# Optimization experiments

Hardware: AMD Instinct MI355X
Metric: run time of the kernel (lower is better)

## Reference

```python
import jax, jax.numpy as jnp
from jax import lax
import numpy as np

D = 1024   # d_model
N = 64     # d_state
P = 64     # headdim
H = 16     # nheads = d_inner // headdim (d_inner = d_model)
E = 8      # n_experts
R = 8      # LoRA rank
OM = 32    # omega_dim
MEMD = 384 # memory vector dim
KC = 4     # d_conv
Bz, Lz = 2, 1024


def setup_inputs() -> dict:
    key = jax.random.key(0)
    it = iter(jax.random.split(key, 48))
    def nrm(shape, s=0.02):
        return jax.random.normal(next(it), shape, jnp.float32) * s
    return dict(
        x=jax.random.normal(next(it), (Bz, Lz, D), jnp.float32),
        wkv_state=nrm((Bz, N, N), 0.1),
        x_prev=jax.random.normal(next(it), (Bz, 1, D), jnp.float32),
        memory_vec=jax.random.normal(next(it), (Bz, MEMD), jnp.float32),
        rag_state=nrm((Bz, N, N), 0.1),
        ssd_state=nrm((Bz, H, P, N), 0.1),
        conv_state=nrm((Bz, D, KC), 0.1),
        norm_scale=jnp.ones((D,), jnp.float32), norm_bias=jnp.zeros((D,), jnp.float32),
        W_in=nrm((2 * D, D)), conv_w=nrm((D, KC), 0.1), conv_b=jnp.zeros((D,), jnp.float32),
        W_dt=nrm((H, D)), dt_bias=jnp.full((H,), -2.0, jnp.float32),
        A_log=jnp.log(jnp.linspace(0.5, 8.0, H)).astype(jnp.float32),
        W_B=nrm((N, D)), W_C=nrm((N, D)), W_ssd_out=nrm((D, D)),
        W_r=nrm((N, D)), W_k=nrm((N, D)), W_v=nrm((N, D)), W_w=nrm((N, D)),
        W_rwkv_out=nrm((D, N)),
        W_skew=nrm((OM, OM), 0.1), W_om_in=nrm((OM, D)), W_om_out=nrm((D, OM)),
        W_router=nrm((E, D)), lora_A=nrm((E, D, R)), lora_B=nrm((E, R, D)),
        W_nov=nrm((1, 2 * D)), b_nov=jnp.zeros((1,), jnp.float32),
        W_ragq=nrm((N, D)), W_rago=nrm((D, N)),
        W_mq=nrm((MEMD, D)), W_mp=nrm((D, MEMD)),
        W_mg=nrm((1, D + MEMD)), b_mg=jnp.zeros((1,), jnp.float32),
    )


def _layernorm(x, s, b):
    m = x.mean(-1, keepdims=True)
    v = ((x - m) ** 2).mean(-1, keepdims=True)
    return (x - m) * lax.rsqrt(v + 1e-5) * s + b


def _forward(x, wkv_state, x_prev, memory_vec, rag_state, ssd_state, conv_state,
             norm_scale, norm_bias, W_in, conv_w, conv_b, W_dt, dt_bias, A_log,
             W_B, W_C, W_ssd_out, W_r, W_k, W_v, W_w, W_rwkv_out,
             W_skew, W_om_in, W_om_out, W_router, lora_A, lora_B, W_nov, b_nov,
             W_ragq, W_rago, W_mq, W_mp, W_mg, b_mg):
    Bb, Ll, _ = x.shape
    residual = x
    xn = _layernorm(x, norm_scale, norm_bias)
    # ---- TarsCoreBlock: Mamba-2 SSD scan + RWKV-7 wkv scan + gated fusion ----
    zu = xn @ W_in.T
    z, u = zu[..., :D], zu[..., D:]
    # depthwise causal conv1d with rolling conv_state [B, D, KC]
    u_cat = jnp.concatenate([conv_state.transpose(0, 2, 1), u], axis=1)  # [B, KC+L, D]
    acc = conv_b
    for k in range(KC):
        acc = acc + u_cat[:, k:k + Ll, :] * conv_w[:, k]
    uc = jax.nn.silu(acc)
    conv_new = u_cat[:, Ll:, :].transpose(0, 2, 1)
    dt = jax.nn.softplus(xn @ W_dt.T + dt_bias)   # [B,L,H]
    A = -jnp.exp(A_log)                            # [H], negative decay rates
    Bm = xn @ W_B.T                                # [B,L,N]
    Cm = xn @ W_C.T                                # [B,L,N]
    uh = uc.reshape(Bb, Ll, H, P)
    def ssd_step(h, inp):
        dt_t, u_t, b_t, c_t = inp                  # [B,H],[B,H,P],[B,N],[B,N]
        h = h * jnp.exp(dt_t * A)[..., None, None] + (dt_t[..., None, None] * u_t[..., None]) * b_t[:, None, None, :]
        return h, jnp.einsum('bhpn,bn->bhp', h, c_t)
    ssd_new, ys = lax.scan(ssd_step, ssd_state,
                           (dt.transpose(1, 0, 2), uh.transpose(1, 0, 2, 3),
                            Bm.transpose(1, 0, 2), Cm.transpose(1, 0, 2)))
    y_ssd = ys.transpose(1, 0, 2, 3).reshape(Bb, Ll, D) @ W_ssd_out.T
    # RWKV-7 style wkv recurrence with time-shift mixing
    x_shift = jnp.concatenate([x_prev, xn[:, :-1]], axis=1)
    mix = 0.5 * (xn + x_shift)
    r, kk, v = mix @ W_r.T, mix @ W_k.T, mix @ W_v.T
    w = jnp.exp(-jnp.exp(mix @ W_w.T))             # per-channel decay in (0,1)
    def rwkv_step(S, inp):
        r_t, k_t, v_t, w_t = inp
        S = S * w_t[:, :, None] + v_t[:, :, None] * k_t[:, None, :]
        return S, jnp.einsum('bij,bj->bi', S, r_t)
    wkv_new, yr = lax.scan(rwkv_step, wkv_state,
                           (r.transpose(1, 0, 2), kk.transpose(1, 0, 2),
                            v.transpose(1, 0, 2), w.transpose(1, 0, 2)))
    y_rwkv = yr.transpose(1, 0, 2) @ W_rwkv_out.T
    core_out = jax.nn.silu(z) * y_ssd + y_rwkv     # WuNeng fusion
    x1 = residual + core_out
    x_prev_new = xn[:, -1:, :]
    # ---- RAG injection from compressed rag_state ----
    q = x1.mean(1) @ W_ragq.T                      # [B,N]
    info = jnp.einsum('bij,bj->bi', rag_state, q)
    x1 = x1 + 0.1 * (info @ W_rago.T)[:, None, :]
    # ---- Omega-SSM: Cayley SO(n) rotation in omega subspace ----
    Ask = 0.5 * (W_skew - W_skew.T)
    I = jnp.eye(OM, dtype=x.dtype)
    Qc = jnp.linalg.solve(I - Ask, I + Ask)        # orthogonal via Cayley map
    x1 = x1 + ((x1 @ W_om_in.T) @ Qc.T) @ W_om_out.T
    # ---- MoLE: sparse top-2 low-rank (LoRA) experts ----
    probs = jax.nn.softmax(x1 @ W_router.T, axis=-1)  # [B,L,E]
    _, topi = lax.top_k(probs, 2)
    mask = jax.nn.one_hot(topi, E, dtype=x.dtype).sum(-2)
    gate = probs * mask
    gate = gate / (gate.sum(-1, keepdims=True) + 1e-9)
    down = jnp.einsum('bld,edr->bler', x1, lora_A)    # [B,L,E,R]
    x2 = x1 + jnp.einsum('bler,erd->bld', down * gate[..., None], lora_B)
    aux = E * jnp.sum(probs.mean((0, 1)) * mask.mean((0, 1)))
    # ---- NoveltyGate blended residual ----
    h_old, h_new = residual.mean(1), x2.mean(1)
    novelty = jax.nn.sigmoid(jnp.concatenate([h_old, h_new], -1) @ W_nov.T + b_nov)[:, 0]
    n = novelty[:, None, None]
    x3 = n * x2 + (1.0 - n) * residual
    # ---- Cosine-gated memory fusion ----
    h_post = x3.mean(1)
    hq = h_post @ W_mq.T
    sim = (hq * memory_vec).sum(-1) / (jnp.linalg.norm(hq, axis=-1) * jnp.linalg.norm(memory_vec, axis=-1) + 1e-8)
    gm = jax.nn.sigmoid(jnp.concatenate([h_post, memory_vec], -1) @ W_mg.T + b_mg)[:, 0]
    x4 = x3 + (sim * gm)[:, None, None] * (memory_vec @ W_mp.T)[:, None, :]
    return x4, wkv_new, x_prev_new, ssd_new, conv_new, aux


def reference(x, wkv_state, x_prev, memory_vec, rag_state, ssd_state, conv_state,
              norm_scale, norm_bias, W_in, conv_w, conv_b, W_dt, dt_bias, A_log,
              W_B, W_C, W_ssd_out, W_r, W_k, W_v, W_w, W_rwkv_out,
              W_skew, W_om_in, W_om_out, W_router, lora_A, lora_B, W_nov, b_nov,
              W_ragq, W_rago, W_mq, W_mp, W_mg, b_mg):
    return _forward(x, wkv_state, x_prev, memory_vec, rag_state, ssd_state, conv_state,
                    norm_scale, norm_bias, W_in, conv_w, conv_b, W_dt, dt_bias, A_log,
                    W_B, W_C, W_ssd_out, W_r, W_k, W_v, W_w, W_rwkv_out,
                    W_skew, W_om_in, W_om_out, W_router, lora_A, lora_B, W_nov, b_nov,
                    W_ragq, W_rago, W_mq, W_mp, W_mg, b_mg)
```

## Files before the change

kernel.cpp:

```cpp
#include <hip/hip_runtime.h>
#include <hip/hip_bf16.h>

#define DD    1024
#define NN    64
#define HH    16
#define EE    8
#define OMM   32
#define MEMDD 384
#define BB    2
#define LL    1024
#define TT    2048

#define OFF_X4    0
#define OFF_WKV   2097152
#define OFF_XPREV 2105344
#define OFF_SSD   2107392
#define OFF_CONV  2238464
#define OFF_AUX   2246656

typedef unsigned short u16;
typedef __attribute__((ext_vector_type(8))) short short8;
typedef __attribute__((ext_vector_type(4))) float f32x4;

__device__ __forceinline__ float us2f(u16 u){ return __uint_as_float(((unsigned)u)<<16); }
__device__ __forceinline__ u16 f2us(float f){
    unsigned u = __float_as_uint(f);
    unsigned r = 0x7FFFu + ((u>>16)&1u);
    return (u16)((u + r) >> 16);
}
__device__ __forceinline__ float LD(const void* p, size_t i, int m){
    return m ? ((const float*)p)[i] : us2f(((const u16*)p)[i]);
}
__device__ __forceinline__ void ST(void* p, size_t i, float v, int m){
    if (m) ((float*)p)[i] = v; else ((u16*)p)[i] = f2us(v);
}
__device__ __forceinline__ float sigf(float x){ return 1.f/(1.f+expf(-x)); }

__device__ __forceinline__ void gl_lds16(const u16* g, u16* l){
    __builtin_amdgcn_global_load_lds((const __attribute__((address_space(1))) void*)g,
                                     (__attribute__((address_space(3))) void*)l,
                                     16, 0, 0);
}

__device__ __forceinline__ float wave_sum64(float v){
    #pragma unroll
    for (int off=32; off>0; off>>=1) v += __shfl_xor(v, off);
    return v;
}
__device__ __forceinline__ float block_sum256(float v, float* red){
    int tid = threadIdx.x;
    red[tid] = v; __syncthreads();
    #pragma unroll
    for (int st=128; st>0; st>>=1){ if (tid<st) red[tid]+=red[tid+st]; __syncthreads(); }
    float r = red[0]; __syncthreads();
    return r;
}
__device__ __forceinline__ int detect_mode(const void* nscale){
    return (((const unsigned*)nscale)[0] == 0x3F800000u) ? 1 : 0;
}
__device__ __forceinline__ void cvt8(const void* src, size_t i, u16* dst, int md){
    if (md){
        float4 a = *(const float4*)((const float*)src + i);
        float4 b = *(const float4*)((const float*)src + i + 4);
        dst[0]=f2us(a.x); dst[1]=f2us(a.y); dst[2]=f2us(a.z); dst[3]=f2us(a.w);
        dst[4]=f2us(b.x); dst[5]=f2us(b.y); dst[6]=f2us(b.z); dst[7]=f2us(b.w);
    } else {
        *(short8*)dst = *(const short8*)((const u16*)src + i);
    }
}

__global__ __launch_bounds__(256)
void prep_k(const void* nscale, int* flag, float* mean1, float* hold, float* hnew,
            const void* W_in, u16* wbfin,
            const void* W_ssd_out, u16* wbfss,
            const void* W_rwkv_out, u16* wbfrw,
            const void* WB, const void* WC, const void* Wdt, u16* wcatxn,
            const void* Wr, const void* Wk, const void* Wv, const void* Ww, u16* wcatmix,
            const void* memv, const void* W_mp, float* mdel){
    __shared__ float mv[MEMDD];
    const int md = detect_mode(nscale);
    int bx = blockIdx.x, tid = threadIdx.x;
    switch (blockIdx.y){
    case 0: {
        size_t i = (size_t)bx*2048 + tid*8;
        cvt8(W_in, i, wbfin + i, md);
    } break;
    case 1: {
        if (bx >= 512) return;
        size_t i = (size_t)bx*2048 + tid*8;
        cvt8(W_ssd_out, i, wbfss + i, md);
    } break;
    case 2: {
        if (bx >= 32) return;
        size_t i = (size_t)bx*2048 + tid*8;
        cvt8(W_rwkv_out, i, wbfrw + i, md);
    } break;
    case 3: {
        if (bx >= 72) return;
        const void* src; size_t off;
        if (bx < 32){ src = WB; off = (size_t)bx*2048; }
        else if (bx < 64){ src = WC; off = (size_t)(bx-32)*2048; }
        else { src = Wdt; off = (size_t)(bx-64)*2048; }
        size_t dsto = (bx < 32) ? off : (bx < 64 ? 65536 + off : 131072 + off);
        cvt8(src, off + tid*8, wcatxn + dsto + tid*8, md);
    } break;
    case 4: {
        if (bx >= 128) return;
        int sel = bx >> 5;
        const void* src = (sel==0)?Wr:(sel==1)?Wk:(sel==2)?Wv:Ww;
        size_t off = (size_t)(bx & 31)*2048 + tid*8;
        cvt8(src, off, wcatmix + (size_t)sel*65536 + off, md);
    } break;
    case 5: {
        if (bx >= 64) return;
        int b = bx & 1, r0 = (bx >> 1)*32;
        int wid = tid >> 6, lane = tid & 63;
        for (int i=tid; i<MEMDD; i+=256) mv[i] = LD(memv, b*MEMDD + i, md);
        __syncthreads();
        #pragma unroll
        for (int rr=0; rr<8; ++rr){
            int row = r0 + wid*8 + rr;
            float s = 0.f;
            size_t wo = (size_t)row*MEMDD;
            #pragma unroll
            for (int it=0; it<6; ++it) s += LD(W_mp, wo + it*64 + lane, md) * mv[it*64 + lane];
            s = wave_sum64(s);
            if (lane == 0) mdel[b*DD + row] = s;
        }
    } break;
    default: {
        if (bx >= 8) return;
        int t = bx*256 + tid;
        if (t == 0) flag[0] = md;
        if (t < BB*DD){ mean1[t]=0.f; hold[t]=0.f; hnew[t]=0.f; }
    } break;
    }
}

__global__ __launch_bounds__(256)
void ln_k(const void* __restrict__ x, const void* __restrict__ scale, const void* __restrict__ bias,
          float* __restrict__ xn, u16* __restrict__ xnbf, void* __restrict__ out, const int* modep){
    __shared__ float red[256];
    const int m = *modep;
    int t = blockIdx.x, tid = threadIdx.x;
    int b = t >> 10, l = t & 1023;
    float v[4]; float s=0.f;
    #pragma unroll
    for (int i=0;i<4;i++){ v[i] = LD(x, (size_t)t*DD + i*256 + tid, m); s += v[i]; }
    float mean = block_sum256(s, red) * (1.f/DD);
    float s2=0.f;
    #pragma unroll
    for (int i=0;i<4;i++){ float d=v[i]-mean; s2 += d*d; }
    float var = block_sum256(s2, red) * (1.f/DD);
    float rstd = rsqrtf(var + 1e-5f);
    #pragma unroll
    for (int i=0;i<4;i++){
        int d = i*256+tid;
        float o = (v[i]-mean)*rstd*LD(scale,d,m) + LD(bias,d,m);
        xn[(size_t)t*DD + d] = o;
        xnbf[(size_t)t*DD + d] = f2us(o);
        if (l == LL-1) ST(out, OFF_XPREV + b*DD + d, o, m);
    }
}

__device__ __forceinline__ void gemm_body(u16* Asm, u16* Bsm,
                const u16* __restrict__ A, const u16* __restrict__ W,
                float* __restrict__ C0, float* __restrict__ C1,
                int N, int K, int Nsplit, int addto, int c0bf, int bx, int by){
    int tid = threadIdx.x;
    int wid = tid >> 6, lane = tid & 63;
    int l15 = lane & 15, quad = lane >> 4;
    int wr = wid >> 1, wc = wid & 1;
    int bm = bx*64, bn = by*128;
    int lr = lane >> 3;
    int lc8 = (lane & 7)*8;
    const u16* Ag = A + (size_t)bm*K;
    const u16* Wg = W + (size_t)bn*K;
    f32x4 acc[2][4];
    #pragma unroll
    for (int m=0;m<2;++m)
        #pragma unroll
        for (int n=0;n<4;++n) acc[m][n] = (f32x4){0.f,0.f,0.f,0.f};
    for (int k0=0; k0<K; k0+=64){
        #pragma unroll
        for (int i=0;i<2;++i){
            int row = wid*16 + i*8 + lr;
            gl_lds16(Ag + (size_t)row*K + k0 + lc8, &Asm[(wid*16 + i*8)*64]);
        }
        #pragma unroll
        for (int i=0;i<4;++i){
            int row = wid*32 + i*8 + lr;
            gl_lds16(Wg + (size_t)row*K + k0 + lc8, &Bsm[(wid*32 + i*8)*64]);
        }
        __syncthreads();
        #pragma unroll
        for (int ks=0; ks<2; ++ks){
            short8 af[2], bf[4];
            #pragma unroll
            for (int m=0;m<2;++m)
                af[m] = *(const short8*)&Asm[(wr*32 + m*16 + l15)*64 + ks*32 + quad*8];
            #pragma unroll
            for (int n=0;n<4;++n)
                bf[n] = *(const short8*)&Bsm[(wc*64 + n*16 + l15)*64 + ks*32 + quad*8];
            #pragma unroll
            for (int m=0;m<2;++m)
                #pragma unroll
                for (int n=0;n<4;++n)
                    acc[m][n] = __builtin_amdgcn_mfma_f32_16x16x32_bf16(af[m], bf[n], acc[m][n], 0,0,0);
        }
        __syncthreads();
    }
    int ns1 = N - Nsplit;
    #pragma unroll
    for (int m=0;m<2;++m){
        #pragma unroll
        for (int n=0;n<4;++n){
            int col = bn + wc*64 + n*16 + l15;
            #pragma unroll
            for (int i=0;i<4;++i){
                int row = bm + wr*32 + m*16 + quad*4 + i;
                float v = acc[m][n][i];
                if (col < Nsplit){
                    size_t id = (size_t)row*Nsplit + col;
                    if (c0bf) ((u16*)C0)[id] = f2us(v);
                    else C0[id] = (addto ? C0[id] : 0.f) + v;
                } else {
                    size_t id = (size_t)row*ns1 + (col - Nsplit);
                    C1[id] = v;
                }
            }
        }
    }
}

__global__ __launch_bounds__(256)
void gemm_big_k(const u16* __restrict__ A, const u16* __restrict__ W,
                float* __restrict__ C0, float* __restrict__ C1,
                int N, int K, int Nsplit, int addto){
    __shared__ u16 Asm[64*64];
    __shared__ u16 Bsm[128*64];
    gemm_body(Asm, Bsm, A, W, C0, C1, N, K, Nsplit, addto, 0, blockIdx.x, blockIdx.y);
}

__global__ __launch_bounds__(256)
void proj_dual_k(const u16* __restrict__ xnbf, const u16* __restrict__ wcatxn,
                 float* __restrict__ pcat2_as_f, float* __restrict__ dtraw,
                 const u16* __restrict__ mixbf, const u16* __restrict__ wcatmix,
                 float* __restrict__ rkvw){
    __shared__ u16 Asm[64*64];
    __shared__ u16 Bsm[128*64];
    if (blockIdx.y < 2)
        gemm_body(Asm, Bsm, xnbf, wcatxn, pcat2_as_f, dtraw, 256, 1024, 128, 0, 1, blockIdx.x, blockIdx.y);
    else
        gemm_body(Asm, Bsm, mixbf, wcatmix, rkvw, dtraw, 256, 1024, 256, 0, 0, blockIdx.x, blockIdx.y-2);
}

__global__ __launch_bounds__(256)
void out_dual_k(const u16* __restrict__ ysbf, const u16* __restrict__ wbfss, float* __restrict__ s1,
                const u16* __restrict__ ybf, const u16* __restrict__ wbfrw, float* __restrict__ s2){
    __shared__ u16 Asm[64*64];
    __shared__ u16 Bsm[128*64];
    if (blockIdx.y < 8)
        gemm_body(Asm, Bsm, ysbf, wbfss, s1, (float*)nullptr, 1024, 1024, 1024, 0, 0, blockIdx.x, blockIdx.y);
    else
        gemm_body(Asm, Bsm, ybf, wbfrw, s2, (float*)nullptr, 1024, 64, 1024, 0, 0, blockIdx.x, blockIdx.y-8);
}

__global__ __launch_bounds__(256)
void cmx_k(const float* __restrict__ u, const float* __restrict__ xn,
           const void* __restrict__ cs, const void* __restrict__ cw, const void* __restrict__ cb,
           const void* __restrict__ xprev,
           float* __restrict__ uc, u16* __restrict__ mixbf, void* __restrict__ out,
           const int* modep){
    const int m = *modep;
    int idx = blockIdx.x*256 + threadIdx.x;
    int t = idx >> 10, d = idx & 1023;
    int b = t >> 10, l = t & 1023;
    float acc = LD(cb, d, m);
    #pragma unroll
    for (int k=0;k<4;++k){
        int i = l + k;
        float xv = (i < 4) ? LD(cs, ((size_t)(b*DD + d))*4 + i, m)
                           : u[(size_t)(t + k - 4)*DD + d];
        acc += xv * LD(cw, d*4 + k, m);
    }
    uc[idx] = acc * sigf(acc);
    float xc = xn[idx];
    float xp = (l == 0) ? LD(xprev, (size_t)b*DD + d, m) : xn[idx - DD];
    mixbf[idx] = f2us(0.5f*(xc + xp));
    if (l >= LL-4)
        ST(out, OFF_CONV + (size_t)b*DD*4 + d*4 + (l - (LL-4)), u[idx], m);
}

#define LDSS 72
__global__ __launch_bounds__(256)
void ssdA_k(const u16* __restrict__ pcat2, const float* __restrict__ dtraw,
            const float* __restrict__ uc,
            const void* __restrict__ A_log, const void* __restrict__ dt_bias,
            float* __restrict__ ys, float* __restrict__ Scb, float* __restrict__ cumsb,
            const int* modep){
    __shared__ u16 Bs[64*LDSS];
    __shared__ u16 Cs[64*LDSS];
    __shared__ u16 BTw[64*LDSS];
    __shared__ u16 XTs[64*LDSS];
    __shared__ float cums[64];
    __shared__ float dts_raw[64];
    const int m = *modep;
    int tid = threadIdx.x;
    int wid = tid >> 6, lane = tid & 63;
    int blk = blockIdx.x;
    int b = blk >> 8, h = (blk >> 4) & 15, c = blk & 15;
    int l16 = lane & 15, quad = lane >> 4;
    int r = tid >> 2;
    int cb4 = (tid & 3) * 16;
    float Ah = -expf(LD(A_log, h, m));
    int t0 = c*64;
    const u16* Pg = pcat2 + (size_t)(b*LL + t0)*128;
    #pragma unroll
    for (int i=0;i<4;++i){
        int cc = cb4 + i*4;
        ushort4 f = *(const ushort4*)(Pg + (size_t)r*128 + cc);
        u16* d1 = &Bs[r*LDSS + cc];
        d1[0]=f.x; d1[1]=f.y; d1[2]=f.z; d1[3]=f.w;
        ushort4 g = *(const ushort4*)(Pg + (size_t)r*128 + 64 + cc);
        u16* d2 = &Cs[r*LDSS + cc];
        d2[0]=g.x; d2[1]=g.y; d2[2]=g.z; d2[3]=g.w;
    }
// ... 52 lines not shown
        for (int i=0;i<4;++i){
            int t_loc = wid*16 + quad*4 + i;
            float gv = (s_loc <= t_loc) ? gacc[nt][i]*expf(cums[t_loc]-cums[s_loc]) : 0.f;
            Bs[t_loc*LDSS + s_loc] = f2us(gv);
        }
    }
    __syncthreads();
    f32x4 acc2[4], acc4[4];
    #pragma unroll
    for (int nt=0;nt<4;++nt){ acc2[nt]=(f32x4){0.f,0.f,0.f,0.f}; acc4[nt]=(f32x4){0.f,0.f,0.f,0.f}; }
    #pragma unroll
    for (int ks=0; ks<64; ks+=32){
        short8 sf = *(const short8*)&Bs[(wid*16 + l16)*LDSS + ks + quad*8];
        short8 xf = *(const short8*)&XTs[(wid*16 + l16)*LDSS + ks + quad*8];
        #pragma unroll
        for (int nt=0;nt<4;++nt){
            short8 xo = *(const short8*)&XTs[(nt*16 + l16)*LDSS + ks + quad*8];
            acc2[nt] = __builtin_amdgcn_mfma_f32_16x16x32_bf16(sf, xo, acc2[nt], 0,0,0);
            short8 bo = *(const short8*)&BTw[(nt*16 + l16)*LDSS + ks + quad*8];
            acc4[nt] = __builtin_amdgcn_mfma_f32_16x16x32_bf16(xf, bo, acc4[nt], 0,0,0);
        }
    }
    #pragma unroll
    for (int nt=0;nt<4;++nt){
        int col = nt*16 + l16;
        #pragma unroll
        for (int i=0;i<4;++i){
            int row = wid*16 + quad*4 + i;
            ys[(size_t)(b*LL + t0 + row)*DD + h*64 + col] = acc2[nt][i];
            Scb[(size_t)blk*4096 + row*64 + col] = acc4[nt][i];
        }
    }
}

#define FS 68
__global__ __launch_bounds__(256)
void rwkvA_k(const float* __restrict__ rkvw,
             float* __restrict__ yr, float* __restrict__ Slb, float* __restrict__ Wcumb){
    __shared__ float wch[64*FS], vch[64*FS], kch[64*FS], rch[64*FS];
    __shared__ float Wc[64*FS];
    __shared__ float part[4*8*64];
    int tid = threadIdx.x;
    int wid = tid >> 6, lane = tid & 63;
    int blk = blockIdx.x;
    int b = blk >> 4, c = blk & 15;
    int t0 = c*64;
    int r = tid >> 2, c4 = (tid & 3)*16;
    const float* base = rkvw + (size_t)(b*LL + t0)*256;
    #pragma unroll
    for (int i=0;i<4;++i){
        int cc = c4 + i*4;
        *(float4*)&rch[r*FS+cc] = *(const float4*)(base + (size_t)r*256 + cc);
        *(float4*)&kch[r*FS+cc] = *(const float4*)(base + (size_t)r*256 + 64 + cc);
        *(float4*)&vch[r*FS+cc] = *(const float4*)(base + (size_t)r*256 + 128 + cc);
        float4 wv = *(const float4*)(base + (size_t)r*256 + 192 + cc);
        wch[r*FS+cc+0] = expf(-expf(wv.x));
        wch[r*FS+cc+1] = expf(-expf(wv.y));
        wch[r*FS+cc+2] = expf(-expf(wv.z));
        wch[r*FS+cc+3] = expf(-expf(wv.w));
    }
    __syncthreads();
    if (wid == 0){
        float cum = 1.f;
        for (int t=0;t<64;++t){ cum *= wch[t*FS+lane]; Wc[t*FS+lane] = cum; }
    }
    __syncthreads();
    #pragma unroll
    for (int q=0;q<16;++q){
        int idx = q*256 + tid;
        int t = idx >> 6, i = idx & 63;
        Wcumb[(size_t)blk*4096 + idx] = Wc[t*FS + i];
    }
    float S[16];
    #pragma unroll
    for (int jj=0;jj<16;++jj) S[jj]=0.f;
    int jb = wid*16;
    for (int t8=0; t8<8; ++t8){
        float ya[8];
        #pragma unroll
        for (int u=0;u<8;++u){
            int t = t8*8+u;
            float wv = wch[t*FS+lane];
            float vv = vch[t*FS+lane];
            float y = 0.f;
            #pragma unroll
            for (int jj=0;jj<16;++jj){
                float kk = kch[t*FS + jb + jj];
                float rr = rch[t*FS + jb + jj];
                S[jj] = S[jj]*wv + vv*kk;
                y += S[jj]*rr;
            }
            ya[u] = y;
        }
        #pragma unroll
        for (int u=0;u<8;++u) part[wid*512 + u*64 + lane] = ya[u];
        __syncthreads();
        #pragma unroll
        for (int it=0; it<2; ++it){
            int e = it*256 + tid;
            int u = e >> 6, i = e & 63;
            float y = part[0*512 + u*64 + i] + part[1*512 + u*64 + i]
                    + part[2*512 + u*64 + i] + part[3*512 + u*64 + i];
            yr[(size_t)(b*LL + t0 + t8*8 + u)*NN + i] = y;
        }
        __syncthreads();
    }
    #pragma unroll
    for (int jj=0;jj<16;++jj)
        Slb[(size_t)blk*4096 + (size_t)lane*64 + jb + jj] = S[jj];
}

__global__ __launch_bounds__(256)
void sb_k(const void* __restrict__ ssd_state, const float* __restrict__ Scb,
          const float* __restrict__ cumsb, u16* __restrict__ hinb,
          const void* __restrict__ wkv_state, const float* __restrict__ Slb,
          const float* __restrict__ Wcumb, u16* __restrict__ hinr,
          void* __restrict__ out, const int* modep){
    const int m = *modep;
    int tid = threadIdx.x;
    if (blockIdx.x < 32){
        int bh = blockIdx.x;
        float h[16];
        #pragma unroll
        for (int i=0;i<16;++i)
            h[i] = LD(ssd_state, (size_t)bh*4096 + i*256 + tid, m);
        for (int c=0; c<16; ++c){
            int blk = bh*16 + c;
            float efull = expf(cumsb[(size_t)blk*64 + 63]);
            #pragma unroll
            for (int i=0;i<16;++i){
                hinb[(size_t)blk*4096 + i*256 + tid] = f2us(h[i]);
                h[i] = efull*h[i] + Scb[(size_t)blk*4096 + i*256 + tid];
            }
        }
        #pragma unroll
        for (int i=0;i<16;++i)
            ST(out, OFF_SSD + (size_t)bh*4096 + i*256 + tid, h[i], m);
    } else {
        int b = blockIdx.x - 32;
        float S[16];
        #pragma unroll
        for (int q=0;q<16;++q)
            S[q] = LD(wkv_state, (size_t)b*4096 + q*256 + tid, m);
        for (int c=0;c<16;++c){
            int blk = b*16+c;
            #pragma unroll
            for (int q=0;q<16;++q){
                int idx = q*256+tid;
                int i = idx >> 6;
                hinr[(size_t)blk*4096 + idx] = f2us(S[q]);
                float P = Wcumb[(size_t)blk*4096 + 63*64 + i];
                S[q] = S[q]*P + Slb[(size_t)blk*4096 + idx];
            }
        }
        #pragma unroll
        for (int q=0;q<16;++q)
            ST(out, OFF_WKV + (size_t)b*4096 + q*256 + tid, S[q], m);
    }
}

__global__ __launch_bounds__(256)
void sc_k(const u16* __restrict__ pcat2, const u16* __restrict__ hinb,
          const float* __restrict__ cumsb, const float* __restrict__ ys, u16* __restrict__ ysbf,
          const float* __restrict__ rkvw, const u16* __restrict__ hinr,
          const float* __restrict__ Wcumb, const float* __restrict__ yr, u16* __restrict__ ybf){
    __shared__ u16 T0[64*LDSS];
    __shared__ u16 T1[64*LDSS];
    int tid = threadIdx.x;
    int wid = tid >> 6, lane = tid & 63;
    int l16 = lane & 15, quad = lane >> 4;
    int r = tid >> 2;
    int cb4 = (tid & 3)*16;
    if (blockIdx.x < 512){
        int blk = blockIdx.x;
        int b = blk >> 8, h = (blk >> 4) & 15, c = blk & 15;
// ... 76 lines not shown
}

__global__ __launch_bounds__(256)
void fuse_mean_k(const float* __restrict__ z, const float* __restrict__ s1,
                 const float* __restrict__ s2, const void* __restrict__ xin,
                 float* __restrict__ x1, float* __restrict__ mean1, const int* modep){
    const int m = *modep;
    int bid = blockIdx.x;
    int lc = bid & 15, dc = (bid >> 4) & 3, b = bid >> 6;
    int d = dc*256 + threadIdx.x;
    float sum = 0.f;
    int l0 = lc*64;
    for (int l=l0; l<l0+64; ++l){
        size_t idx = (size_t)(b*LL + l)*DD + d;
        float zl = z[idx];
        float v = LD(xin, idx, m) + zl*sigf(zl)*s1[idx] + s2[idx];
        x1[idx] = v;
        sum += v;
    }
    atomicAdd(&mean1[b*DD + d], sum*(1.f/LL));
}

__global__ __launch_bounds__(256)
void ragA_k(const float* __restrict__ mean1, const void* __restrict__ W_ragq,
            float* __restrict__ qb, const int* modep){
    const int m = *modep;
    int bx = blockIdx.x;
    int b = bx >> 4;
    int tid = threadIdx.x, wid = tid >> 6, lane = tid & 63;
    int row = (bx & 15)*4 + wid;
    float s = 0.f;
    size_t wo = (size_t)row*DD;
    #pragma unroll
    for (int it=0; it<16; ++it)
        s += LD(W_ragq, wo + it*64 + lane, m) * mean1[(b<<10) + it*64 + lane];
    s = wave_sum64(s);
    if (lane == 0) qb[b*64 + row] = s;
}

__global__ __launch_bounds__(256)
void ragB_k(const float* __restrict__ qb, const void* __restrict__ rag_state,
            float* __restrict__ infob, const int* modep){
    const int m = *modep;
    int bx = blockIdx.x;
    int b = bx >> 4;
    int tid = threadIdx.x, wid = tid >> 6, lane = tid & 63;
    int row = (bx & 15)*4 + wid;
    float s = LD(rag_state, (size_t)(b*64+row)*64 + lane, m) * qb[b*64 + lane];
    s = wave_sum64(s);
    if (lane == 0) infob[b*64 + row] = s;
}

__global__ __launch_bounds__(256)
void ragC_k(const float* __restrict__ infob, const void* __restrict__ W_rago,
            float* __restrict__ ragd, const int* modep){
    const int m = *modep;
    int bx = blockIdx.x;
    int b = bx >> 6;
    int tid = threadIdx.x, wid = tid >> 6, lane = tid & 63;
    int r0 = (bx & 63)*16 + wid*4;
    float iv = infob[b*64 + lane];
    #pragma unroll
    for (int rr=0; rr<4; ++rr){
        int d = r0 + rr;
        float s = iv * LD(W_rago, (size_t)d*64 + lane, m);
        s = wave_sum64(s);
        if (lane == 0) ragd[(b<<10) + d] = 0.1f*s;
    }
}

__global__ __launch_bounds__(256)
void addrag_k(float* __restrict__ x1, const float* __restrict__ ragd, u16* __restrict__ xbf){
    int i4 = (blockIdx.x*256 + threadIdx.x)*4;
    int b = i4 >> 20, d = i4 & 1023;
    #pragma unroll
    for (int j=0;j<4;++j){
        float v = x1[i4+j] + ragd[(b<<10) + d + j];
        x1[i4+j] = v;
        xbf[i4+j] = f2us(v);
    }
}

__global__ __launch_bounds__(256)
void cayley_k(const void* __restrict__ W_skew, float* __restrict__ Qc, const int* modep){
    __shared__ float Aug[32][65];
    __shared__ float fac[32];
    const int m = *modep;
    int tid = threadIdx.x;
    for (int idx = tid; idx < 1024; idx += 256){
        int r = idx >> 5, c = idx & 31;
        float a = 0.5f*(LD(W_skew, r*32+c, m) - LD(W_skew, c*32+r, m));
        float eye = (r==c) ? 1.f : 0.f;
        Aug[r][c] = eye - a;
        Aug[r][32+c] = eye + a;
    }
    __syncthreads();
    for (int p=0; p<32; ++p){
        float inv = 1.f / Aug[p][p];
        __syncthreads();
        if (tid < 64) Aug[p][tid] *= inv;
        if (tid < 32 && tid != p) fac[tid] = Aug[tid][p];
        __syncthreads();
        for (int idx = tid; idx < 2048; idx += 256){
            int r = idx >> 6, c = idx & 63;
            if (r != p) Aug[r][c] -= fac[r]*Aug[p][c];
        }
        __syncthreads();
    }
    for (int idx = tid; idx < 1024; idx += 256){
        int r = idx >> 5, c = idx & 31;
        Qc[idx] = Aug[r][32+c];
    }
}

__global__ __launch_bounds__(256)
void wcomb2_k(const void* __restrict__ W_om_out, const float* __restrict__ Qc,
              const void* __restrict__ W_om_in, u16* __restrict__ wcomb, const int* modep){
    const int md = *modep;
    int d = blockIdx.x;
    int tid = threadIdx.x;
    __shared__ float qc[1024];
    __shared__ float wrow[32];
    __shared__ float trow[32];
    #pragma unroll
    for (int i=0;i<4;i++) qc[i*256+tid] = Qc[i*256+tid];
    if (tid < 32) wrow[tid] = LD(W_om_out, (size_t)d*OMM + tid, md);
    __syncthreads();
    if (tid < 32){
        float s = 0.f;
        #pragma unroll
        for (int j=0;j<32;++j) s += wrow[j]*qc[j*32 + tid];
        trow[tid] = s;
    }
    __syncthreads();
    #pragma unroll
    for (int p=0; p<4; ++p){
        int e = p*256 + tid;
        float s = 0.f;
        #pragma unroll
        for (int k=0; k<32; ++k) s += trow[k] * LD(W_om_in, (size_t)k*DD + e, md);
        wcomb[(size_t)d*DD + e] = f2us(s);
    }
}

__global__ __launch_bounds__(256)
void moe_k(const float* __restrict__ x1, const void* __restrict__ W_router,
           const void* __restrict__ lora_A, const void* __restrict__ lora_B,
           float* __restrict__ x2, float* __restrict__ probs8, int* __restrict__ eidx,
           const int* modep){
    const int m = *modep;
    int t = blockIdx.x, tid = threadIdx.x;
    int wid = tid >> 6, lane = tid & 63;
    __shared__ float xs[1024];
    __shared__ float red[32];
    __shared__ float logits[8];
    __shared__ float downs[16];
    __shared__ float gsh[2];
    __shared__ int esh[2];
    #pragma unroll
    for (int i=0;i<4;i++) xs[i*256+tid] = x1[(size_t)t*DD + i*256+tid];
    __syncthreads();
    {
        float p0=0.f, p1=0.f;
        size_t w0o = (size_t)(2*wid)*DD, w1o = (size_t)(2*wid+1)*DD;
        #pragma unroll
        for (int it=0; it<16; ++it){
            float xv = xs[it*64 + lane];
            p0 += xv * LD(W_router, w0o + it*64 + lane, m);
            p1 += xv * LD(W_router, w1o + it*64 + lane, m);
        }
        p0 = wave_sum64(p0); p1 = wave_sum64(p1);
        if (lane == 0){ logits[2*wid] = p0; logits[2*wid+1] = p1; }
    }
    __syncthreads();
    if (tid == 0){
        float mx = logits[0];
        for (int e2=1;e2<8;++e2) mx = fmaxf(mx, logits[e2]);
        float pe[8]; float sum=0.f;
        for (int e2=0;e2<8;++e2){ pe[e2]=expf(logits[e2]-mx); sum+=pe[e2]; }
        for (int e2=0;e2<8;++e2) pe[e2] /= sum;
        int e0=0; for (int e2=1;e2<8;++e2) if (pe[e2]>pe[e0]) e0=e2;
        int e1=(e0==0)?1:0; for (int e2=0;e2<8;++e2) if (e2!=e0 && pe[e2]>pe[e1]) e1=e2;
        float gs = pe[e0]+pe[e1]+1e-9f;
        gsh[0]=pe[e0]/gs; gsh[1]=pe[e1]/gs; esh[0]=e0; esh[1]=e1;
        #pragma unroll
        for (int e2=0;e2<8;++e2) probs8[(size_t)t*8 + e2] = pe[e2];
        eidx[t*2+0]=e0; eidx[t*2+1]=e1;
    }
    __syncthreads();
    {
        int ei = wid & 1, half = wid >> 1;
        int e2 = esh[ei];
        int dsub = lane >> 3;
        size_t ao = (size_t)e2*8192 + (size_t)half*4096;
        float acc = 0.f;
        #pragma unroll
        for (int c=0; c<64; ++c){
            float xv = xs[half*512 + c*8 + dsub];
            acc += xv * LD(lora_A, ao + c*64 + lane, m);
        }
        acc += __shfl_xor(acc, 8);
        acc += __shfl_xor(acc, 16);
        acc += __shfl_xor(acc, 32);
        if (lane < 8) red[wid*8 + lane] = acc;
    }
    __syncthreads();
    if (tid < 16){
        int ei = tid >> 3, r = tid & 7;
        downs[ei*8 + r] = red[ei*8 + r] + red[(ei+2)*8 + r];
    }
    __syncthreads();
    {
        int e0=esh[0], e1=esh[1]; float g0=gsh[0], g1=gsh[1];
        #pragma unroll
        for (int i=0;i<4;i++){
            int d = i*256+tid;
            float acc=0.f;
            size_t b0 = (size_t)e0*8192 + d;
            size_t b1 = (size_t)e1*8192 + d;
            #pragma unroll
            for (int r=0;r<8;++r) acc += g0*downs[r]*LD(lora_B, b0 + (size_t)r*1024, m)
                                       + g1*downs[8+r]*LD(lora_B, b1 + (size_t)r*1024, m);
            x2[(size_t)t*DD + d] = xs[d] + acc;
        }
    }
}

__global__ __launch_bounds__(256)
void colmean2_k(const float* __restrict__ x2, const void* __restrict__ xin,
                float* __restrict__ hnew, float* __restrict__ hold, const int* modep){
    const int m = *modep;
    int bid = blockIdx.x;
    int lc = bid & 15, dc = (bid >> 4) & 3, b = bid >> 6;
    int d = dc*256 + threadIdx.x;
    float s = 0.f;
    int l0 = lc*64;
    if (blockIdx.y == 0){
        for (int l=l0; l<l0+64; ++l) s += x2[(size_t)(b*LL + l)*DD + d];
        atomicAdd(&hnew[b*DD + d], s*(1.f/LL));
    } else {
        for (int l=l0; l<l0+64; ++l) s += LD(xin, (size_t)(b*LL + l)*DD + d, m);
        atomicAdd(&hold[b*DD + d], s*(1.f/LL));
    }
}

__global__ __launch_bounds__(256)
void hq2_k(const float* __restrict__ hold, const float* __restrict__ hnew,
           const void* __restrict__ W_nov, const void* __restrict__ b_nov,
           const void* __restrict__ W_mq, float* __restrict__ hqb, const int* modep){
    const int m = *modep;
    int b = blockIdx.x, tid = threadIdx.x;
    int wid = tid >> 6, lane = tid & 63;
    int r0 = blockIdx.y*16;
    __shared__ float hs[1024];
    __shared__ float red[256];
    float p=0.f;
    #pragma unroll
    for (int i=0;i<4;i++){ int d=i*256+tid;
        p += hold[b*DD+d]*LD(W_nov,d,m) + hnew[b*DD+d]*LD(W_nov,DD+d,m); }
    float n = sigf(block_sum256(p, red) + LD(b_nov,0,m));
    #pragma unroll
    for (int i=0;i<4;i++){ int d=i*256+tid;
        hs[d] = n*hnew[b*DD+d] + (1.f-n)*hold[b*DD+d]; }
    __syncthreads();
    #pragma unroll
    for (int rr=0; rr<4; ++rr){
        int row = r0 + wid*4 + rr;
        float s = 0.f;
        size_t wo = (size_t)row*DD;
        #pragma unroll
        for (int it=0; it<16; ++it) s += LD(W_mq, wo + it*64 + lane, m) * hs[it*64 + lane];
        s = wave_sum64(s);
        if (lane == 0) hqb[b*MEMDD + row] = s;
    }
}

__global__ __launch_bounds__(256)
void gate2_k(const float* __restrict__ hold, const float* __restrict__ hnew,
             const void* __restrict__ W_nov, const void* __restrict__ b_nov,
             const float* __restrict__ hqb, const void* __restrict__ memv,
             const void* __restrict__ W_mg, const void* __restrict__ b_mg,
             const float* __restrict__ probs8, const int* __restrict__ eidx,
             float* __restrict__ scal, void* __restrict__ out, const int* modep){
    const int m = *modep;
    int b = blockIdx.x, tid = threadIdx.x;
    __shared__ float red[256];
    float p=0.f;
    #pragma unroll
    for (int i=0;i<4;i++){ int d=i*256+tid;
        p += hold[b*DD+d]*LD(W_nov,d,m) + hnew[b*DD+d]*LD(W_nov,DD+d,m); }
    float n = sigf(block_sum256(p, red) + LD(b_nov,0,m));
    float pn=0.f, ph=0.f, pm=0.f;
    for (int mm=tid; mm<MEMDD; mm+=256){
        float mv = LD(memv, b*MEMDD+mm, m);
        float h = hqb[b*MEMDD+mm];
        pn += h*mv; ph += h*h; pm += mv*mv;
    }
    float num = block_sum256(pn, red);
    float nh  = block_sum256(ph, red);
    float nm  = block_sum256(pm, red);
    float sim = num / (sqrtf(nh)*sqrtf(nm) + 1e-8f);
    float pg=0.f;
    #pragma unroll
    for (int i=0;i<4;i++){ int d=i*256+tid;
        float hp = n*hnew[b*DD+d] + (1.f-n)*hold[b*DD+d];
        pg += hp*LD(W_mg,d,m); }
    for (int mm=tid; mm<MEMDD; mm+=256) pg += LD(memv,b*MEMDD+mm,m)*LD(W_mg,DD+mm,m);
    float gdot = block_sum256(pg, red) + LD(b_mg,0,m);
    float gm = sigf(gdot);
    if (tid==0){ scal[b] = n; scal[2+b] = sim*gm; }
    if (b == 0){
        float ps[8] = {0.f,0.f,0.f,0.f,0.f,0.f,0.f,0.f};
        float cs[8] = {0.f,0.f,0.f,0.f,0.f,0.f,0.f,0.f};
        for (int t=tid; t<TT; t+=256){
            #pragma unroll
            for (int e=0;e<8;++e) ps[e] += probs8[(size_t)t*8 + e];
            int e0 = eidx[t*2], e1 = eidx[t*2+1];
            #pragma unroll
            for (int e=0;e<8;++e) cs[e] += (e0==e ? 1.f : 0.f) + (e1==e ? 1.f : 0.f);
        }
        float aux = 0.f;
        #pragma unroll
        for (int e=0;e<8;++e){
            float sp = block_sum256(ps[e], red);
            float sc = block_sum256(cs[e], red);
            aux += (sp*(1.f/TT))*(sc*(1.f/TT));
        }
        if (tid==0) ST(out, OFF_AUX, 8.f*aux, m);
    }
}

__global__ __launch_bounds__(256)
void final_k(const float* __restrict__ x2, const void* __restrict__ xin,
             const float* __restrict__ scal, const float* __restrict__ mdelta,
             void* __restrict__ out, const int* modep){
    const int m = *modep;
    int i4 = (blockIdx.x*256 + threadIdx.x)*4;
    int b = i4 >> 20, d = i4 & 1023;
    float n = scal[b], coef = scal[2+b];
    #pragma unroll
    for (int j=0;j<4;++j){
        float v = n*x2[i4+j] + (1.f-n)*LD(xin,i4+j,m) + coef*mdelta[(b<<10)+d+j];
        ST(out, OFF_X4 + i4 + j, v, m);
    }
}

extern "C" void kernel_launch(void* const* d_in, const int* in_sizes, int n_in,
                              void* d_out, int out_size, void* d_ws, size_t ws_size,
                              hipStream_t stream){
    typedef const void* cb;
    cb x         = d_in[0];
    cb wkv_state = d_in[1];
    cb x_prev    = d_in[2];
    cb memv      = d_in[3];
    cb rag_state = d_in[4];
    cb ssd_state = d_in[5];
    cb conv_state= d_in[6];
    cb nscale    = d_in[7];
    cb nbias     = d_in[8];
    cb W_in      = d_in[9];
    cb conv_w    = d_in[10];
    cb conv_b    = d_in[11];
    cb W_dt      = d_in[12];
    cb dt_bias   = d_in[13];
    cb A_log     = d_in[14];
    cb W_B       = d_in[15];
    cb W_C       = d_in[16];
    cb W_ssd_out = d_in[17];
    cb W_r       = d_in[18];
    cb W_k       = d_in[19];
    cb W_v       = d_in[20];
    cb W_w       = d_in[21];
    cb W_rwkv_out= d_in[22];
    cb W_skew    = d_in[23];
    cb W_om_in   = d_in[24];
    cb W_om_out  = d_in[25];
    cb W_router  = d_in[26];
    cb lora_A    = d_in[27];
    cb lora_B    = d_in[28];
    cb W_nov     = d_in[29];
    cb b_nov     = d_in[30];
    cb W_ragq    = d_in[31];
    cb W_rago    = d_in[32];
    cb W_mq      = d_in[33];
    cb W_mp      = d_in[34];
    cb W_mg      = d_in[35];
    cb b_mg      = d_in[36];

    float* ws = (float*)d_ws;
    size_t o = 0;
    float* xn_x1   = ws + o; o += (size_t)TT*DD;
    float* z_x2    = ws + o; o += (size_t)TT*DD;
    float* u_ys    = ws + o; o += (size_t)TT*DD;
    float* ucb     = ws + o; o += (size_t)TT*DD;
    float* s2b     = ws + o; o += (size_t)TT*DD;
    float* dtraw   = ws + o; o += (size_t)TT*128;
    float* rkvw    = ws + o; o += (size_t)TT*256;
    float* yrb     = ws + o; o += (size_t)TT*NN;
    float* Qcb     = ws + o; o += 1024;
    float* Scb     = ws + o; o += (size_t)512*4096;
    float* cumsb   = ws + o; o += (size_t)512*64;
    float* Wcumb   = ws + o; o += (size_t)32*4096;
    float* Slb     = ws + o; o += (size_t)32*4096;
    u16*   hinb    = (u16*)(ws + o); o += (size_t)512*4096/2;
    u16*   hinr    = (u16*)(ws + o); o += (size_t)32*4096/2;
    float* mean1   = ws + o; o += BB*DD;
    float* ragd    = ws + o; o += BB*DD;
    float* qb      = ws + o; o += BB*NN;
    float* infob   = ws + o; o += BB*NN;
    float* holdb   = ws + o; o += BB*DD;
    float* hnewb   = ws + o; o += BB*DD;
    float* scal    = ws + o; o += 16;
    float* mdel    = ws + o; o += BB*DD;
    float* hqb     = ws + o; o += BB*MEMDD;
    float* probs8  = ws + o; o += (size_t)TT*8;
    int*   eidx    = (int*)(ws + o); o += (size_t)TT*2;
    int*   flag    = (int*)(ws + o); o += 16;
    u16*   xnbf    = (u16*)(ws + o); o += (size_t)TT*DD/2;
    u16*   mixbf   = (u16*)(ws + o); o += (size_t)TT*DD/2;
    u16*   x1bf    = (u16*)(ws + o); o += (size_t)TT*DD/2;
    u16*   ysbf    = (u16*)(ws + o); o += (size_t)TT*DD/2;
    u16*   ybf     = (u16*)(ws + o); o += (size_t)TT*NN/2;
    u16*   pcat2   = (u16*)(ws + o); o += (size_t)TT*128/2;
    u16*   wbfin   = (u16*)(ws + o); o += (size_t)2*DD*DD/2;
    u16*   wbfss   = (u16*)(ws + o); o += (size_t)DD*DD/2;
    u16*   wbfrw   = (u16*)(ws + o); o += (size_t)DD*NN/2;
    u16*   wcatxn  = (u16*)(ws + o); o += (size_t)256*DD/2;
    u16*   wcatmix = (u16*)(ws + o); o += (size_t)256*DD/2;
    u16*   wcombbf = (u16*)(ws + o); o += (size_t)DD*DD/2;

    dim3 blk(256);

    hipLaunchKernelGGL(prep_k, dim3(1024,7), blk, 0, stream,
                       nscale, flag, mean1, holdb, hnewb,
                       W_in, wbfin, W_ssd_out, wbfss, W_rwkv_out, wbfrw,
                       W_B, W_C, W_dt, wcatxn, W_r, W_k, W_v, W_w, wcatmix,
                       memv, W_mp, mdel);
    hipLaunchKernelGGL(cayley_k, dim3(1), blk, 0, stream, W_skew, Qcb, flag);
    hipLaunchKernelGGL(wcomb2_k, dim3(1024), blk, 0, stream, W_om_out, Qcb, W_om_in, wcombbf, flag);
    hipLaunchKernelGGL(ln_k, dim3(TT), blk, 0, stream, x, nscale, nbias, xn_x1, xnbf, d_out, flag);
    hipLaunchKernelGGL(gemm_big_k, dim3(TT/64, 16), blk, 0, stream, xnbf, wbfin,
                       z_x2, u_ys, 2*DD, DD, DD, 0);
    hipLaunchKernelGGL(cmx_k, dim3(TT*DD/256), blk, 0, stream, u_ys, xn_x1,
                       conv_state, conv_w, conv_b, x_prev, ucb, mixbf, d_out, flag);
    hipLaunchKernelGGL(proj_dual_k, dim3(TT/64, 4), blk, 0, stream,
                       xnbf, wcatxn, (float*)pcat2, dtraw, mixbf, wcatmix, rkvw);
    hipLaunchKernelGGL(ssdA_k, dim3(512), blk, 0, stream, pcat2, dtraw, ucb, A_log, dt_bias,
                       u_ys , Scb, cumsb, flag);
    hipLaunchKernelGGL(rwkvA_k, dim3(32), blk, 0, stream, rkvw, yrb, Slb, Wcumb);
    hipLaunchKernelGGL(sb_k, dim3(34), blk, 0, stream, ssd_state, Scb, cumsb, hinb,
                       wkv_state, Slb, Wcumb, hinr, d_out, flag);
    hipLaunchKernelGGL(sc_k, dim3(544), blk, 0, stream, pcat2, hinb, cumsb, u_ys, ysbf,
                       rkvw, hinr, Wcumb, yrb, ybf);
    hipLaunchKernelGGL(out_dual_k, dim3(TT/64, 16), blk, 0, stream,
                       ysbf, wbfss, ucb , ybf, wbfrw, s2b);
    hipLaunchKernelGGL(fuse_mean_k, dim3(128), blk, 0, stream, z_x2, ucb, s2b, x,
                       xn_x1 , mean1, flag);
    hipLaunchKernelGGL(ragA_k, dim3(32), blk, 0, stream, mean1, W_ragq, qb, flag);
    hipLaunchKernelGGL(ragB_k, dim3(32), blk, 0, stream, qb, rag_state, infob, flag);
    hipLaunchKernelGGL(ragC_k, dim3(128), blk, 0, stream, infob, W_rago, ragd, flag);
    hipLaunchKernelGGL(addrag_k, dim3(TT*DD/1024), blk, 0, stream, xn_x1, ragd, x1bf);
    hipLaunchKernelGGL(gemm_big_k, dim3(TT/64, 8), blk, 0, stream, x1bf, wcombbf,
                       xn_x1, (float*)nullptr, DD, DD, DD, 1);
    hipLaunchKernelGGL(moe_k, dim3(TT), blk, 0, stream, xn_x1, W_router, lora_A, lora_B, z_x2,
                       probs8, eidx, flag);
    hipLaunchKernelGGL(colmean2_k, dim3(128,2), blk, 0, stream, z_x2, x, hnewb, holdb, flag);
    hipLaunchKernelGGL(hq2_k, dim3(BB,24), blk, 0, stream, holdb, hnewb, W_nov, b_nov,
                       W_mq, hqb, flag);
    hipLaunchKernelGGL(gate2_k, dim3(BB), blk, 0, stream, holdb, hnewb, W_nov, b_nov,
                       hqb, memv, W_mg, b_mg, probs8, eidx, scal, d_out, flag);
    hipLaunchKernelGGL(final_k, dim3(TT*DD/1024), blk, 0, stream, z_x2, x, scal, mdel, d_out, flag);
}
```

Measured before the change: 474.9 us.

## Fold Cayley and wcomb into prep/LN kernels, add 128x128 input GEMM

The single-block Cayley inverse moves into prep_k as an extra grid row, and the wcomb computation is appended to ln_k as extra blocks, which removes two kernel launches. The input projection switches to a new 128x128-tile MFMA GEMM that gets more reuse per loaded tile. The RWKV inner loop is split into four independent accumulators to shorten the dependency chain, and the aux-loss reduction uses wave reductions in place of sixteen block reductions. Putting the serial Cayley solve inside prep_k may lengthen that kernel's tail, and the larger GEMM tiles launch fewer blocks.

After: 461.5 us. 1.03x faster.

```diff
diff --git a/kernel.cpp b/kernel.cpp
--- a/kernel.cpp
+++ b/kernel.cpp
@@ -76,8 +76,11 @@
             const void* W_rwkv_out, u16* wbfrw,
             const void* WB, const void* WC, const void* Wdt, u16* wcatxn,
             const void* Wr, const void* Wk, const void* Wv, const void* Ww, u16* wcatmix,
-            const void* memv, const void* W_mp, float* mdel){
+            const void* memv, const void* W_mp, float* mdel,
+            const void* W_skew, float* Qc){
     __shared__ float mv[MEMDD];
+    __shared__ float Aug[32][65];
+    __shared__ float fac[32];
     const int md = detect_mode(nscale);
     int bx = blockIdx.x, tid = threadIdx.x;
     switch (blockIdx.y){
@@ -128,6 +131,33 @@
             if (lane == 0) mdel[b*DD + row] = s;
         }
     } break;
+    case 6: {
+        if (bx >= 1) return;
+        for (int idx = tid; idx < 1024; idx += 256){
+            int r = idx >> 5, c = idx & 31;
+            float a = 0.5f*(LD(W_skew, r*32+c, md) - LD(W_skew, c*32+r, md));
+            float eye = (r==c) ? 1.f : 0.f;
+            Aug[r][c] = eye - a;
+            Aug[r][32+c] = eye + a;
+        }
+        __syncthreads();
+        for (int p=0; p<32; ++p){
+            float inv = 1.f / Aug[p][p];
+            __syncthreads();
+            if (tid < 64) Aug[p][tid] *= inv;
+            if (tid < 32 && tid != p) fac[tid] = Aug[tid][p];
+            __syncthreads();
+            for (int idx = tid; idx < 2048; idx += 256){
+                int r = idx >> 6, c = idx & 63;
+                if (r != p) Aug[r][c] -= fac[r]*Aug[p][c];
+            }
+            __syncthreads();
+        }
+        for (int idx = tid; idx < 1024; idx += 256){
+            int r = idx >> 5, c = idx & 31;
+            Qc[idx] = Aug[r][32+c];
+        }
+    } break;
     default: {
         if (bx >= 8) return;
         int t = bx*256 + tid;
@@ -139,10 +169,40 @@
 
 __global__ __launch_bounds__(256)
 void ln_k(const void* __restrict__ x, const void* __restrict__ scale, const void* __restrict__ bias,
-          float* __restrict__ xn, u16* __restrict__ xnbf, void* __restrict__ out, const int* modep){
+          float* __restrict__ xn, u16* __restrict__ xnbf, void* __restrict__ out,
+          const void* __restrict__ W_om_out, const float* __restrict__ Qc,
+          const void* __restrict__ W_om_in, u16* __restrict__ wcomb,
+          const int* modep){
     __shared__ float red[256];
-    const int m = *modep;
-    int t = blockIdx.x, tid = threadIdx.x;
+    __shared__ float qc[1024];
+    __shared__ float wrow[32];
+    __shared__ float trow[32];
+    const int m = *modep;
+    int bx = blockIdx.x, tid = threadIdx.x;
+    if (bx >= TT){
+        int d = bx - TT;
+        #pragma unroll
+        for (int i=0;i<4;i++) qc[i*256+tid] = Qc[i*256+tid];
+        if (tid < 32) wrow[tid] = LD(W_om_out, (size_t)d*OMM + tid, m);
+        __syncthreads();
+        if (tid < 32){
+            float s = 0.f;
+            #pragma unroll
+            for (int j=0;j<32;++j) s += wrow[j]*qc[j*32 + tid];
+            trow[tid] = s;
+        }
+        __syncthreads();
+        #pragma unroll
+        for (int p=0; p<4; ++p){
+            int e = p*256 + tid;
+            float s = 0.f;
+            #pragma unroll
+            for (int k=0; k<32; ++k) s += trow[k] * LD(W_om_in, (size_t)k*DD + e, m);
+            wcomb[(size_t)d*DD + e] = f2us(s);
+        }
+        return;
+    }
+    int t = bx;
     int b = t >> 10, l = t & 1023;
     float v[4]; float s=0.f;
     #pragma unroll
@@ -243,6 +303,75 @@
 }
 
 __global__ __launch_bounds__(256)
+void gemm_big2_k(const u16* __restrict__ A, const u16* __restrict__ W,
+                 float* __restrict__ C0, float* __restrict__ C1,
+                 int N, int K, int Nsplit){
+    __shared__ u16 Asm[128*64];
+    __shared__ u16 Bsm[128*64];
+    int tid = threadIdx.x;
+    int wid = tid >> 6, lane = tid & 63;
+    int l15 = lane & 15, quad = lane >> 4;
+    int wr = wid >> 1, wc = wid & 1;
+    int bm = blockIdx.x*128, bn = blockIdx.y*128;
+    int lr = lane >> 3;
+    int lc8 = (lane & 7)*8;
+    const u16* Ag = A + (size_t)bm*K;
+    const u16* Wg = W + (size_t)bn*K;
+    f32x4 acc[4][4];
+    #pragma unroll
+    for (int m=0;m<4;++m)
+        #pragma unroll
+        for (int n=0;n<4;++n) acc[m][n] = (f32x4){0.f,0.f,0.f,0.f};
+    for (int k0=0; k0<K; k0+=64){
+        #pragma unroll
+        for (int i=0;i<4;++i){
+            int row = wid*32 + i*8 + lr;
+            gl_lds16(Ag + (size_t)row*K + k0 + lc8, &Asm[(wid*32 + i*8)*64]);
+        }
+        #pragma unroll
+        for (int i=0;i<4;++i){
+            int row = wid*32 + i*8 + lr;
+            gl_lds16(Wg + (size_t)row*K + k0 + lc8, &Bsm[(wid*32 + i*8)*64]);
+        }
+        __syncthreads();
+        #pragma unroll
+        for (int ks=0; ks<2; ++ks){
+            short8 af[4], bf[4];
+            #pragma unroll
+            for (int m=0;m<4;++m)
+                af[m] = *(const short8*)&Asm[(wr*64 + m*16 + l15)*64 + ks*32 + quad*8];
+            #pragma unroll
+            for (int n=0;n<4;++n)
+                bf[n] = *(const short8*)&Bsm[(wc*64 + n*16 + l15)*64 + ks*32 + quad*8];
+            #pragma unroll
+            for (int m=0;m<4;++m)
+                #pragma unroll
+                for (int n=0;n<4;++n)
+                    acc[m][n] = __builtin_amdgcn_mfma_f32_16x16x32_bf16(af[m], bf[n], acc[m][n], 0,0,0);
+        }
+        __syncthreads();
+    }
+    int ns1 = N - Nsplit;
+    #pragma unroll
+    for (int m=0;m<4;++m){
+        #pragma unroll
+        for (int n=0;n<4;++n){
+            int col = bn + wc*64 + n*16 + l15;
+            #pragma unroll
+            for (int i=0;i<4;++i){
+                int row = bm + wr*64 + m*16 + quad*4 + i;
+                float v = acc[m][n][i];
+                if (col < Nsplit){
+                    C0[(size_t)row*Nsplit + col] = v;
+                } else {
+                    C1[(size_t)row*ns1 + (col - Nsplit)] = v;
+                }
+            }
+        }
+    }
+}
+
+__global__ __launch_bounds__(256)
 void proj_dual_k(const u16* __restrict__ xnbf, const u16* __restrict__ wcatxn,
                  float* __restrict__ pcat2_as_f, float* __restrict__ dtraw,
                  const u16* __restrict__ mixbf, const u16* __restrict__ wcatmix,
@@ -461,15 +590,19 @@
             int t = t8*8+u;
             float wv = wch[t*FS+lane];
             float vv = vch[t*FS+lane];
-            float y = 0.f;
-            #pragma unroll
-            for (int jj=0;jj<16;++jj){
-                float kk = kch[t*FS + jb + jj];
-                float rr = rch[t*FS + jb + jj];
-                S[jj] = S[jj]*wv + vv*kk;
-                y += S[jj]*rr;
+            float yy0=0.f, yy1=0.f, yy2=0.f, yy3=0.f;
+            #pragma unroll
+            for (int jj=0;jj<16;jj+=4){
+                float k0v = kch[t*FS + jb + jj+0], r0v = rch[t*FS + jb + jj+0];
+                float k1v = kch[t*FS + jb + jj+1], r1v = rch[t*FS + jb + jj+1];
+                float k2v = kch[t*FS + jb + jj+2], r2v = rch[t*FS + jb + jj+2];
+                float k3v = kch[t*FS + jb + jj+3], r3v = rch[t*FS + jb + jj+3];
+                S[jj+0] = S[jj+0]*wv + vv*k0v; yy0 += S[jj+0]*r0v;
+                S[jj+1] = S[jj+1]*wv + vv*k1v; yy1 += S[jj+1]*r1v;
+                S[jj+2] = S[jj+2]*wv + vv*k2v; yy2 += S[jj+2]*r2v;
+                S[jj+3] = S[jj+3]*wv + vv*k3v; yy3 += S[jj+3]*r3v;
             }
-            ya[u] = y;
+            ya[u] = (yy0+yy1)+(yy2+yy3);
         }
         #pragma unroll
         for (int u=0;u<8;++u) part[wid*512 + u*64 + lane] = ya[u];
@@ -712,68 +845,6 @@
 }
 
 __global__ __launch_bounds__(256)
-void cayley_k(const void* __restrict__ W_skew, float* __restrict__ Qc, const int* modep){
-    __shared__ float Aug[32][65];
-    __shared__ float fac[32];
-    const int m = *modep;
-    int tid = threadIdx.x;
-    for (int idx = tid; idx < 1024; idx += 256){
-        int r = idx >> 5, c = idx & 31;
-        float a = 0.5f*(LD(W_skew, r*32+c, m) - LD(W_skew, c*32+r, m));
-        float eye = (r==c) ? 1.f : 0.f;
-        Aug[r][c] = eye - a;
-        Aug[r][32+c] = eye + a;
-    }
-    __syncthreads();
-    for (int p=0; p<32; ++p){
-        float inv = 1.f / Aug[p][p];
-        __syncthreads();
-        if (tid < 64) Aug[p][tid] *= inv;
-        if (tid < 32 && tid != p) fac[tid] = Aug[tid][p];
-        __syncthreads();
-        for (int idx = tid; idx < 2048; idx += 256){
-            int r = idx >> 6, c = idx & 63;
-            if (r != p) Aug[r][c] -= fac[r]*Aug[p][c];
-        }
-        __syncthreads();
-    }
-    for (int idx = tid; idx < 1024; idx += 256){
-        int r = idx >> 5, c = idx & 31;
-        Qc[idx] = Aug[r][32+c];
-    }
-}
-
-__global__ __launch_bounds__(256)
-void wcomb2_k(const void* __restrict__ W_om_out, const float* __restrict__ Qc,
-              const void* __restrict__ W_om_in, u16* __restrict__ wcomb, const int* modep){
-    const int md = *modep;
-    int d = blockIdx.x;
-    int tid = threadIdx.x;
-    __shared__ float qc[1024];
-    __shared__ float wrow[32];
-    __shared__ float trow[32];
-    #pragma unroll
-    for (int i=0;i<4;i++) qc[i*256+tid] = Qc[i*256+tid];
-    if (tid < 32) wrow[tid] = LD(W_om_out, (size_t)d*OMM + tid, md);
-    __syncthreads();
-    if (tid < 32){
-        float s = 0.f;
-        #pragma unroll
-        for (int j=0;j<32;++j) s += wrow[j]*qc[j*32 + tid];
-        trow[tid] = s;
-    }
-    __syncthreads();
-    #pragma unroll
-    for (int p=0; p<4; ++p){
-        int e = p*256 + tid;
-        float s = 0.f;
-        #pragma unroll
-        for (int k=0; k<32; ++k) s += trow[k] * LD(W_om_in, (size_t)k*DD + e, md);
-        wcomb[(size_t)d*DD + e] = f2us(s);
-    }
-}
-
-__global__ __launch_bounds__(256)
 void moe_k(const float* __restrict__ x1, const void* __restrict__ W_router,
            const void* __restrict__ lora_A, const void* __restrict__ lora_B,
            float* __restrict__ x2, float* __restrict__ probs8, int* __restrict__ eidx,
@@ -914,7 +985,10 @@
              float* __restrict__ scal, void* __restrict__ out, const int* modep){
     const int m = *modep;
     int b = blockIdx.x, tid = threadIdx.x;
+    int wid = tid >> 6, lane = tid & 63;
     __shared__ float red[256];
+    __shared__ float rps[4][8];
+    __shared__ float rcs[4][8];
     float p=0.f;
     #pragma unroll
     for (int i=0;i<4;i++){ int d=i*256+tid;
@@ -949,14 +1023,23 @@
             #pragma unroll
             for (int e=0;e<8;++e) cs[e] += (e0==e ? 1.f : 0.f) + (e1==e ? 1.f : 0.f);
         }
-        float aux = 0.f;
         #pragma unroll
         for (int e=0;e<8;++e){
-            float sp = block_sum256(ps[e], red);
-            float sc = block_sum256(cs[e], red);
-            aux += (sp*(1.f/TT))*(sc*(1.f/TT));
-        }
-        if (tid==0) ST(out, OFF_AUX, 8.f*aux, m);
+            float vp = wave_sum64(ps[e]);
+            float vc = wave_sum64(cs[e]);
+            if (lane == 0){ rps[wid][e] = vp; rcs[wid][e] = vc; }
+        }
+        __syncthreads();
+        if (tid==0){
+            float aux = 0.f;
+            #pragma unroll
+            for (int e=0;e<8;++e){
+                float sp = rps[0][e]+rps[1][e]+rps[2][e]+rps[3][e];
+                float sc = rcs[0][e]+rcs[1][e]+rcs[2][e]+rcs[3][e];
+                aux += (sp*(1.f/TT))*(sc*(1.f/TT));
+            }
+            ST(out, OFF_AUX, 8.f*aux, m);
+        }
     }
 }
 
@@ -1061,16 +1144,15 @@
 
     dim3 blk(256);
 
-    hipLaunchKernelGGL(prep_k, dim3(1024,7), blk, 0, stream,
+    hipLaunchKernelGGL(prep_k, dim3(1024,8), blk, 0, stream,
                        nscale, flag, mean1, holdb, hnewb,
                        W_in, wbfin, W_ssd_out, wbfss, W_rwkv_out, wbfrw,
                        W_B, W_C, W_dt, wcatxn, W_r, W_k, W_v, W_w, wcatmix,
-                       memv, W_mp, mdel);
-    hipLaunchKernelGGL(cayley_k, dim3(1), blk, 0, stream, W_skew, Qcb, flag);
-    hipLaunchKernelGGL(wcomb2_k, dim3(1024), blk, 0, stream, W_om_out, Qcb, W_om_in, wcombbf, flag);
-    hipLaunchKernelGGL(ln_k, dim3(TT), blk, 0, stream, x, nscale, nbias, xn_x1, xnbf, d_out, flag);
-    hipLaunchKernelGGL(gemm_big_k, dim3(TT/64, 16), blk, 0, stream, xnbf, wbfin,
-                       z_x2, u_ys, 2*DD, DD, DD, 0);
+                       memv, W_mp, mdel, W_skew, Qcb);
+    hipLaunchKernelGGL(ln_k, dim3(TT + 1024), blk, 0, stream, x, nscale, nbias, xn_x1, xnbf, d_out,
+                       W_om_out, Qcb, W_om_in, wcombbf, flag);
+    hipLaunchKernelGGL(gemm_big2_k, dim3(TT/128, 16), blk, 0, stream, xnbf, wbfin,
+                       z_x2, u_ys, 2*DD, DD, DD);
     hipLaunchKernelGGL(cmx_k, dim3(TT*DD/256), blk, 0, stream, u_ys, xn_x1,
                        conv_state, conv_w, conv_b, x_prev, ucb, mixbf, d_out, flag);
     hipLaunchKernelGGL(proj_dual_k, dim3(TT/64, 4), blk, 0, stream,
```
